# Optimization experiments

Hardware: AMD Instinct MI355X
Metric: run time of the kernel (lower is better)

## Reference

```python
import jax, jax.numpy as jnp
import numpy as np

EMB = 64
HID = 64


def setup_inputs() -> dict:
    key = jax.random.key(0)
    ks = jax.random.split(key, 7)
    obs_len, batch = 20, 65536
    s_in = 1.0 / np.sqrt(2.0)   # torch Linear init scale
    s_h = 1.0 / np.sqrt(HID)    # torch LSTM init scale
    return {
        "obs_traj": jax.random.normal(ks[0], (obs_len, batch, 2), dtype=jnp.float32),
        "W_emb": jax.random.uniform(ks[1], (EMB, 2), jnp.float32, -s_in, s_in),
        "b_emb": jax.random.uniform(ks[2], (EMB,), jnp.float32, -s_in, s_in),
        "W_ih": jax.random.uniform(ks[3], (4 * HID, EMB), jnp.float32, -s_h, s_h),
        "W_hh": jax.random.uniform(ks[4], (4 * HID, HID), jnp.float32, -s_h, s_h),
        "b_ih": jax.random.uniform(ks[5], (4 * HID,), jnp.float32, -s_h, s_h),
        "b_hh": jax.random.uniform(ks[6], (4 * HID,), jnp.float32, -s_h, s_h),
    }


def reference(obs_traj, W_emb, b_emb, W_ih, W_hh, b_ih, b_hh):
    # spatial embedding: (T, B, 2) -> (T, B, EMB)
    emb = jnp.einsum("tbi,ei->tbe", obs_traj, W_emb) + b_emb
    batch = obs_traj.shape[1]
    bias = b_ih + b_hh  # (4H,)
    # precompute input contribution for all timesteps: (T, B, 4H)
    x_gates = jnp.einsum("tbe,ge->tbg", emb, W_ih) + bias

    def step(carry, xg_t):
        h, c = carry
        gates = xg_t + h @ W_hh.T          # (B, 4H)
        i, f, g, o = jnp.split(gates, 4, axis=-1)  # torch gate order i,f,g,o
        i = jax.nn.sigmoid(i)
        f = jax.nn.sigmoid(f)
        g = jnp.tanh(g)
        o = jax.nn.sigmoid(o)
        c_new = f * c + i * g
        h_new = o * jnp.tanh(c_new)
        return (h_new, c_new), None

    h0 = jnp.zeros((batch, HID), dtype=obs_traj.dtype)
    c0 = jnp.zeros((batch, HID), dtype=obs_traj.dtype)
    (h_T, _), _ = jax.lax.scan(step, (h0, c0), x_gates)
    return h_T[None]  # (num_layers=1, batch, h_dim)
```

## Files before the change

### kernel.cpp

```cpp
#include <hip/hip_runtime.h>

#define T_STEPS 20
#define BATCH   65536
#define HIDN    64
#define GATES   256
#define CHUNKS  2
#define HSTR    72

typedef __bf16 bf16x8 __attribute__((ext_vector_type(8)));
typedef float  f32x4  __attribute__((ext_vector_type(4)));
typedef float  f32x2  __attribute__((ext_vector_type(2)));
typedef unsigned int uint32;
typedef uint32 uint32x4 __attribute__((ext_vector_type(4)));

#define L2E 1.4426950408889634f

#if __has_builtin(__builtin_amdgcn_exp2f)
#define EXP2F(x) __builtin_amdgcn_exp2f(x)
#else
#define EXP2F(x) exp2f(x)
#endif
#if __has_builtin(__builtin_amdgcn_rcpf)
#define RCPF(x) __builtin_amdgcn_rcpf(x)
#else
#define RCPF(x) (1.0f / (x))
#endif

__device__ __forceinline__ uint32 pack2bf16(float a, float b) {
    unsigned short ua = __builtin_bit_cast(unsigned short, (__bf16)a);
    unsigned short ub = __builtin_bit_cast(unsigned short, (__bf16)b);
    return (uint32)ua | ((uint32)ub << 16);
}

__global__ __launch_bounds__(256)
__attribute__((amdgpu_waves_per_eu(4, 4)))
void Encoder_6949257085628_kernel(const float* __restrict__ obs,
                                  const float* __restrict__ W_emb,
                                  const float* __restrict__ b_emb,
                                  const float* __restrict__ W_ih,
                                  const float* __restrict__ W_hh,
                                  const float* __restrict__ b_ih,
                                  const float* __restrict__ b_hh,
                                  float* __restrict__ out) {
    __shared__ float wcbc[GATES * 3];
    __shared__ __align__(16) __bf16 hlb[2][32 * HSTR];

    const int tid  = threadIdx.x;
    const int jtw  = tid >> 6;
    const int lane = tid & 63;
    const int q    = lane >> 4;
    const int c16  = lane & 15;
    const bool qz  = (q == 0);

    {
        int g = tid;
        float sf = ((g >> 6) == 2) ? (2.0f * L2E) : (-L2E);
        float a0 = 0.f, a1 = 0.f, ab = 0.f;
        for (int e = 0; e < 64; ++e) {
            float wie = W_ih[g * 64 + e];
            a0 = fmaf(wie, W_emb[e * 2 + 0], a0);
            a1 = fmaf(wie, W_emb[e * 2 + 1], a1);
            ab = fmaf(wie, b_emb[e], ab);
        }
        wcbc[g * 3 + 0] = a0 * sf;
        wcbc[g * 3 + 1] = a1 * sf;
        wcbc[g * 3 + 2] = (ab + b_ih[g] + b_hh[g]) * sf;
    }

    bf16x8 bfr[4][2];
    #pragma unroll
    for (int f = 0; f < 4; ++f) {
        const float sf = (f == 2) ? (2.0f * L2E) : (-L2E);
        const int rowW = f * 64 + jtw * 16 + c16;
        #pragma unroll
        for (int ks = 0; ks < 2; ++ks) {
            const float* p = W_hh + rowW * 64 + ks * 32 + q * 8;
            f32x4 lo = *(const f32x4*)p;
            f32x4 hi = *(const f32x4*)(p + 4);
            bf16x8 b;
            b[0] = (__bf16)(lo[0] * sf); b[1] = (__bf16)(lo[1] * sf);
            b[2] = (__bf16)(lo[2] * sf); b[3] = (__bf16)(lo[3] * sf);
            b[4] = (__bf16)(hi[0] * sf); b[5] = (__bf16)(hi[1] * sf);
            b[6] = (__bf16)(hi[2] * sf); b[7] = (__bf16)(hi[3] * sf);
            bfr[f][ks] = b;
        }
    }
    __syncthreads();

    uint32 bxw0[4], bxw1[4];
    #pragma unroll
    for (int f = 0; f < 4; ++f) {
        int col = f * 64 + jtw * 16 + c16;
        float w0s = wcbc[col * 3 + 0];
        float w1s = wcbc[col * 3 + 1];
        float bcs = wcbc[col * 3 + 2];
        float blo = bcs - (float)((__bf16)bcs);
        bxw0[f] = qz ? pack2bf16(w0s, w1s) : 0u;
        bxw1[f] = qz ? pack2bf16(bcs, blo) : 0u;
    }
    const uint32 axw1 = qz ? 0x3F803F80u : 0u;

    const int wgBase = blockIdx.x * (32 * CHUNKS);
    const int hOff   = jtw * 16 + c16;

    #pragma unroll 1
    for (int c = 0; c < CHUNKS; ++c) {
        const int rbw = wgBase + c * 32;
        __syncthreads();

        f32x2 cst[2][2];
        #pragma unroll
        for (int m = 0; m < 2; ++m)
            #pragma unroll
            for (int rp = 0; rp < 2; ++rp) cst[m][rp] = f32x2{0.f, 0.f};

        f32x2 xc[2];
        #pragma unroll
        for (int m = 0; m < 2; ++m)
            xc[m] = *(const f32x2*)&obs[(size_t)(rbw + m * 16 + c16) * 2];

        auto ax_of = [&](f32x2 xv) -> bf16x8 {
            uint32 w0 = qz ? pack2bf16(xv[0], xv[1]) : 0u;
            return __builtin_bit_cast(bf16x8, uint32x4{w0, axw1, 0u, 0u});
        };
        auto bx_of = [&](int f) -> bf16x8 {
            return __builtin_bit_cast(bf16x8, uint32x4{bxw0[f], bxw1[f], 0u, 0u});
        };
        auto act_store = [&](f32x4 (&acc)[4], int m, __bf16* hw, bool last) {
            #pragma unroll
            for (int rp = 0; rp < 2; ++rp) {
                const int r0 = 2 * rp, r1 = 2 * rp + 1;
                f32x2 A{EXP2F(acc[0][r0]), EXP2F(acc[0][r1])};
                f32x2 E{EXP2F(acc[1][r0]), EXP2F(acc[1][r1])};
                f32x2 B{EXP2F(acc[2][r0]), EXP2F(acc[2][r1])};
                f32x2 C{EXP2F(acc[3][r0]), EXP2F(acc[3][r1])};
                f32x2 one{1.0f, 1.0f};
                f32x2 pA = A + one, pB = B + one, pE = E + one;
                f32x2 P  = pA * pB;
                f32x2 Bm = B - one;
                f32x2 num = __builtin_elementwise_fma(cst[m][rp], P, Bm * pE);
                f32x2 den = pE * P;
                f32x2 rd{RCPF(den[0]), RCPF(den[1])};
                f32x2 cc = num * rd;
                cst[m][rp] = cc;
                f32x2 ccs = cc * f32x2{2.0f * L2E, 2.0f * L2E};
                f32x2 D{EXP2F(ccs[0]), EXP2F(ccs[1])};
                f32x2 hn = D - one;
                f32x2 hd = (one + C) * (one + D);
                f32x2 rh{RCPF(hd[0]), RCPF(hd[1])};
                f32x2 h  = hn * rh;
                if (!last) {
                    hw[(m * 16 + q * 4 + r0) * HSTR + hOff] = (__bf16)h[0];
                    hw[(m * 16 + q * 4 + r1) * HSTR + hOff] = (__bf16)h[1];
                } else {
                    out[(size_t)(rbw + m * 16 + q * 4 + r0) * HIDN + hOff] = h[0];
                    out[(size_t)(rbw + m * 16 + q * 4 + r1) * HIDN + hOff] = h[1];
                }
            }
        };

        bf16x8 a0c[2], a1c[2];

        {
            f32x4 acc[2][4];
            #pragma unroll
            for (int m = 0; m < 2; ++m) {
                bf16x8 ax = ax_of(xc[m]);
                #pragma unroll
                for (int f = 0; f < 4; ++f)
                    acc[m][f] = __builtin_amdgcn_mfma_f32_16x16x32_bf16(
                        ax, bx_of(f), f32x4{0.f, 0.f, 0.f, 0.f}, 0, 0, 0);
            }
            #pragma unroll
            for (int m = 0; m < 2; ++m)
                xc[m] = *(const f32x2*)&obs[(size_t)(BATCH * 2) + (size_t)(rbw + m * 16 + c16) * 2];
            act_store(acc[0], 0, hlb[0], false);
            act_store(acc[1], 1, hlb[0], false);
            __syncthreads();
            #pragma unroll
            for (int m = 0; m < 2; ++m) {
                a0c[m] = *(const bf16x8*)&hlb[0][(m * 16 + c16) * HSTR + q * 8];
                a1c[m] = *(const bf16x8*)&hlb[0][(m * 16 + c16) * HSTR + 32 + q * 8];
            }
        }

        #pragma unroll 1
        for (int t = 1; t < T_STEPS - 1; ++t) {
            f32x4 acc[2][4];
            #pragma unroll
            for (int m = 0; m < 2; ++m) {
                bf16x8 ax = ax_of(xc[m]);
                #pragma unroll
                for (int f = 0; f < 4; ++f) {
                    acc[m][f] = __builtin_amdgcn_mfma_f32_16x16x32_bf16(
                        ax, bx_of(f), f32x4{0.f, 0.f, 0.f, 0.f}, 0, 0, 0);
                    acc[m][f] = __builtin_amdgcn_mfma_f32_16x16x32_bf16(
                        a0c[m], bfr[f][0], acc[m][f], 0, 0, 0);
                    acc[m][f] = __builtin_amdgcn_mfma_f32_16x16x32_bf16(
                        a1c[m], bfr[f][1], acc[m][f], 0, 0, 0);
                }
            }
            #pragma unroll
            for (int m = 0; m < 2; ++m)
                xc[m] = *(const f32x2*)&obs[(size_t)(t + 1) * (BATCH * 2) + (size_t)(rbw + m * 16 + c16) * 2];
            act_store(acc[0], 0, hlb[t & 1], false);
            act_store(acc[1], 1, hlb[t & 1], false);
            __syncthreads();
            #pragma unroll
            for (int m = 0; m < 2; ++m) {
                a0c[m] = *(const bf16x8*)&hlb[t & 1][(m * 16 + c16) * HSTR + q * 8];
                a1c[m] = *(const bf16x8*)&hlb[t & 1][(m * 16 + c16) * HSTR + 32 + q * 8];
            }
        }

        {
            f32x4 acc[2][4];
            #pragma unroll
            for (int m = 0; m < 2; ++m) {
                bf16x8 ax = ax_of(xc[m]);
                #pragma unroll
                for (int f = 0; f < 4; ++f) {
                    acc[m][f] = __builtin_amdgcn_mfma_f32_16x16x32_bf16(
                        ax, bx_of(f), f32x4{0.f, 0.f, 0.f, 0.f}, 0, 0, 0);
                    acc[m][f] = __builtin_amdgcn_mfma_f32_16x16x32_bf16(
                        a0c[m], bfr[f][0], acc[m][f], 0, 0, 0);
                    acc[m][f] = __builtin_amdgcn_mfma_f32_16x16x32_bf16(
                        a1c[m], bfr[f][1], acc[m][f], 0, 0, 0);
                }
            }
            act_store(acc[0], 0, nullptr, true);
            act_store(acc[1], 1, nullptr, true);
        }
    }
}

extern "C" void kernel_launch(void* const* d_in, const int* in_sizes, int n_in,
                              void* d_out, int out_size, void* d_ws, size_t ws_size,
                              hipStream_t stream) {
    const float* obs   = (const float*)d_in[0];
    const float* W_emb = (const float*)d_in[1];
    const float* b_emb = (const float*)d_in[2];
    const float* W_ih  = (const float*)d_in[3];
    const float* W_hh  = (const float*)d_in[4];
    const float* b_ih  = (const float*)d_in[5];
    const float* b_hh  = (const float*)d_in[6];
    float* out = (float*)d_out;

    dim3 grid(BATCH / (32 * CHUNKS));
    dim3 block(256);
    Encoder_6949257085628_kernel<<<grid, block, 0, stream>>>(
        obs, W_emb, b_emb, W_ih, W_hh, b_ih, b_hh, out);
}
```

Before: 103.9 us.

## Software-pipeline input-projection MFMAs one step ahead with ping-pong accumulators

Splits each LSTM step's MFMA work into the input-projection part and the recurrent part. The input part for step t+1 is now issued into a second accumulator set while step t's recurrent MFMAs and activations proceed, and the loop is unrolled by two to alternate accumulators. The goal is to take the input-projection MFMAs off the serial recurrence critical path. In exchange it doubles accumulator register use, which may raise VGPR pressure or reduce occupancy.

```diff
diff --git a/kernel.cpp b/kernel.cpp
--- a/kernel.cpp
+++ b/kernel.cpp
@@ -114,17 +114,50 @@
             #pragma unroll
             for (int rp = 0; rp < 2; ++rp) cst[m][rp] = f32x2{0.f, 0.f};
 
-        f32x2 xc[2];
-        #pragma unroll
-        for (int m = 0; m < 2; ++m)
-            xc[m] = *(const f32x2*)&obs[(size_t)(rbw + m * 16 + c16) * 2];
-
+        f32x2  xc[2];
+        bf16x8 a0c[2], a1c[2];
+        f32x4  accA[2][4], accB[2][4];
+
+        auto loadx = [&](int t) {
+            const float* ob = obs + (size_t)t * (BATCH * 2);
+            #pragma unroll
+            for (int m = 0; m < 2; ++m)
+                xc[m] = *(const f32x2*)&ob[(size_t)(rbw + m * 16 + c16) * 2];
+        };
         auto ax_of = [&](f32x2 xv) -> bf16x8 {
             uint32 w0 = qz ? pack2bf16(xv[0], xv[1]) : 0u;
             return __builtin_bit_cast(bf16x8, uint32x4{w0, axw1, 0u, 0u});
         };
         auto bx_of = [&](int f) -> bf16x8 {
             return __builtin_bit_cast(bf16x8, uint32x4{bxw0[f], bxw1[f], 0u, 0u});
+        };
+        auto xmfma = [&](f32x4 (&acc)[2][4]) {
+            #pragma unroll
+            for (int m = 0; m < 2; ++m) {
+                bf16x8 ax = ax_of(xc[m]);
+                #pragma unroll
+                for (int f = 0; f < 4; ++f)
+                    acc[m][f] = __builtin_amdgcn_mfma_f32_16x16x32_bf16(
+                        ax, bx_of(f), f32x4{0.f, 0.f, 0.f, 0.f}, 0, 0, 0);
+            }
+        };
+        auto hmfma = [&](f32x4 (&acc)[2][4]) {
+            #pragma unroll
+            for (int m = 0; m < 2; ++m)
+                #pragma unroll
+                for (int f = 0; f < 4; ++f) {
+                    acc[m][f] = __builtin_amdgcn_mfma_f32_16x16x32_bf16(
+                        a0c[m], bfr[f][0], acc[m][f], 0, 0, 0);
+                    acc[m][f] = __builtin_amdgcn_mfma_f32_16x16x32_bf16(
+                        a1c[m], bfr[f][1], acc[m][f], 0, 0, 0);
+                }
+        };
+        auto readA = [&](const __bf16* hp) {
+            #pragma unroll
+            for (int m = 0; m < 2; ++m) {
+                a0c[m] = *(const bf16x8*)&hp[(m * 16 + c16) * HSTR + q * 8];
+                a1c[m] = *(const bf16x8*)&hp[(m * 16 + c16) * HSTR + 32 + q * 8];
+            }
         };
         auto act_store = [&](f32x4 (&acc)[4], int m, __bf16* hw, bool last) {
             #pragma unroll
@@ -159,78 +192,37 @@
             }
         };
 
-        bf16x8 a0c[2], a1c[2];
-
-        {
-            f32x4 acc[2][4];
-            #pragma unroll
-            for (int m = 0; m < 2; ++m) {
-                bf16x8 ax = ax_of(xc[m]);
-                #pragma unroll
-                for (int f = 0; f < 4; ++f)
-                    acc[m][f] = __builtin_amdgcn_mfma_f32_16x16x32_bf16(
-                        ax, bx_of(f), f32x4{0.f, 0.f, 0.f, 0.f}, 0, 0, 0);
-            }
-            #pragma unroll
-            for (int m = 0; m < 2; ++m)
-                xc[m] = *(const f32x2*)&obs[(size_t)(BATCH * 2) + (size_t)(rbw + m * 16 + c16) * 2];
-            act_store(acc[0], 0, hlb[0], false);
-            act_store(acc[1], 1, hlb[0], false);
+        loadx(0);
+        xmfma(accA);
+        loadx(1);
+        xmfma(accB);
+        loadx(2);
+        act_store(accA[0], 0, hlb[0], false);
+        act_store(accA[1], 1, hlb[0], false);
+        __syncthreads();
+        readA(hlb[0]);
+
+        #pragma unroll 1
+        for (int tt = 1; tt < T_STEPS - 1; tt += 2) {
+            hmfma(accB);
+            xmfma(accA);
+            loadx(tt + 2 < T_STEPS ? tt + 2 : T_STEPS - 1);
+            act_store(accB[0], 0, hlb[1], false);
+            act_store(accB[1], 1, hlb[1], false);
             __syncthreads();
-            #pragma unroll
-            for (int m = 0; m < 2; ++m) {
-                a0c[m] = *(const bf16x8*)&hlb[0][(m * 16 + c16) * HSTR + q * 8];
-                a1c[m] = *(const bf16x8*)&hlb[0][(m * 16 + c16) * HSTR + 32 + q * 8];
-            }
+            readA(hlb[1]);
+            hmfma(accA);
+            xmfma(accB);
+            loadx(tt + 3 < T_STEPS ? tt + 3 : T_STEPS - 1);
+            act_store(accA[0], 0, hlb[0], false);
+            act_store(accA[1], 1, hlb[0], false);
+            __syncthreads();
+            readA(hlb[0]);
         }
 
-        #pragma unroll 1
-        for (int t = 1; t < T_STEPS - 1; ++t) {
-            f32x4 acc[2][4];
-            #pragma unroll
-            for (int m = 0; m < 2; ++m) {
-                bf16x8 ax = ax_of(xc[m]);
-                #pragma unroll
-                for (int f = 0; f < 4; ++f) {
-                    acc[m][f] = __builtin_amdgcn_mfma_f32_16x16x32_bf16(
-                        ax, bx_of(f), f32x4{0.f, 0.f, 0.f, 0.f}, 0, 0, 0);
-                    acc[m][f] = __builtin_amdgcn_mfma_f32_16x16x32_bf16(
-                        a0c[m], bfr[f][0], acc[m][f], 0, 0, 0);
-                    acc[m][f] = __builtin_amdgcn_mfma_f32_16x16x32_bf16(
-                        a1c[m], bfr[f][1], acc[m][f], 0, 0, 0);
-                }
-            }
-            #pragma unroll
-            for (int m = 0; m < 2; ++m)
-                xc[m] = *(const f32x2*)&obs[(size_t)(t + 1) * (BATCH * 2) + (size_t)(rbw + m * 16 + c16) * 2];
-            act_store(acc[0], 0, hlb[t & 1], false);
-            act_store(acc[1], 1, hlb[t & 1], false);
-            __syncthreads();
-            #pragma unroll
-            for (int m = 0; m < 2; ++m) {
-                a0c[m] = *(const bf16x8*)&hlb[t & 1][(m * 16 + c16) * HSTR + q * 8];
-                a1c[m] = *(const bf16x8*)&hlb[t & 1][(m * 16 + c16) * HSTR + 32 + q * 8];
-            }
-        }
-
-        {
-            f32x4 acc[2][4];
-            #pragma unroll
-            for (int m = 0; m < 2; ++m) {
-                bf16x8 ax = ax_of(xc[m]);
-                #pragma unroll
-                for (int f = 0; f < 4; ++f) {
-                    acc[m][f] = __builtin_amdgcn_mfma_f32_16x16x32_bf16(
-                        ax, bx_of(f), f32x4{0.f, 0.f, 0.f, 0.f}, 0, 0, 0);
-                    acc[m][f] = __builtin_amdgcn_mfma_f32_16x16x32_bf16(
-                        a0c[m], bfr[f][0], acc[m][f], 0, 0, 0);
-                    acc[m][f] = __builtin_amdgcn_mfma_f32_16x16x32_bf16(
-                        a1c[m], bfr[f][1], acc[m][f], 0, 0, 0);
-                }
-            }
-            act_store(acc[0], 0, nullptr, true);
-            act_store(acc[1], 1, nullptr, true);
-        }
+        hmfma(accB);
+        act_store(accB[0], 0, nullptr, true);
+        act_store(accB[1], 1, nullptr, true);
     }
 }
 
```

Result: slower. 166.6 us (+60.4%).
